# Performance work log

Hardware: AMD Instinct MI355X
Metric: run time of the kernel (lower is better)

## Reference

```python
import jax, jax.numpy as jnp
import numpy as np

EMBED = 1024
HEADS = 16
HEAD_DIM = EMBED // HEADS


def setup_inputs() -> dict:
    key = jax.random.key(0)
    ks = jax.random.split(key, 10)
    B, S = 2, 2048
    x = jax.random.normal(ks[0], (B, S, EMBED), dtype=jnp.float32)
    s = 1.0 / np.sqrt(EMBED)
    Wq = jax.random.normal(ks[1], (EMBED, EMBED), dtype=jnp.float32) * s
    Wk = jax.random.normal(ks[2], (EMBED, EMBED), dtype=jnp.float32) * s
    Wv = jax.random.normal(ks[3], (EMBED, EMBED), dtype=jnp.float32) * s
    Wo = jax.random.normal(ks[4], (EMBED, EMBED), dtype=jnp.float32) * s
    bq = jnp.zeros((EMBED,), jnp.float32)
    bk = jnp.zeros((EMBED,), jnp.float32)
    bv = jnp.zeros((EMBED,), jnp.float32)
    bo = jnp.zeros((EMBED,), jnp.float32)
    J = jax.random.normal(ks[5], (HEADS, HEAD_DIM, HEAD_DIM), dtype=jnp.float32) * 0.02
    lam = jnp.asarray(0.5, jnp.float32)
    return {"x": x, "Wq": Wq, "bq": bq, "Wk": Wk, "bk": bk,
            "Wv": Wv, "bv": bv, "Wo": Wo, "bo": bo, "J": J, "lam": lam}


def reference(x, Wq, bq, Wk, bk, Wv, bv, Wo, bo, J, lam):
    B, S, E = x.shape
    H, hd = HEADS, HEAD_DIM
    scale = np.sqrt(hd).astype(np.float32)

    def split_heads(t):  # (B,S,E) -> (B,H,S,hd)
        return t.reshape(B, S, H, hd).transpose(0, 2, 1, 3)

    Q = split_heads(x @ Wq + bq)
    K = split_heads(x @ Wk + bk)
    V = split_heads(x @ Wv + bv)

    scores = jnp.einsum('bhid,bhjd->bhij', Q, K) / scale
    Qn = jnp.tanh(Q)
    Kn = jnp.tanh(K)
    # bilinear correction: tanh(Q) J tanh(K)^T per head
    delta = jnp.einsum('bhid,hde,bhje->bhij', Qn, J, Kn)
    scores = scores + lam * delta

    causal = jnp.triu(jnp.ones((S, S), dtype=bool), k=1)  # True above diagonal
    scores = jnp.where(causal[None, None], -jnp.inf, scores)

    probs = jax.nn.softmax(scores, axis=-1)
    out = jnp.einsum('bhij,bhjd->bhid', probs, V)
    out = out.transpose(0, 2, 1, 3).reshape(B, S, E)
    return out @ Wo + bo
```

## Files before the change

kernel.cpp:

```cpp
#include <hip/hip_runtime.h>
#include <cstdint>
#include <cstddef>

typedef __bf16 bf16x8 __attribute__((ext_vector_type(8)));
typedef short  s16x8  __attribute__((ext_vector_type(8)));
typedef float  f32x4  __attribute__((ext_vector_type(4)));
typedef unsigned int u32x4 __attribute__((ext_vector_type(4)));
typedef unsigned int u32x2 __attribute__((ext_vector_type(2)));

#define MFMA16(a, b, c) __builtin_amdgcn_mfma_f32_16x16x32_bf16((a), (b), (c), 0, 0, 0)

typedef __attribute__((address_space(3))) unsigned int       lds_uint;
typedef const __attribute__((address_space(1))) unsigned int glb_uint;

static __device__ __forceinline__ void gload_lds16(const void* g, void* l) {
  __builtin_amdgcn_global_load_lds((glb_uint*)g, (lds_uint*)l, 16, 0, 0);
}

static __device__ __forceinline__ unsigned short f2bf(float f) {
  unsigned u = __builtin_bit_cast(unsigned, f);
  unsigned r = u + 0x7FFFu + ((u >> 16) & 1u);
  return (unsigned short)(r >> 16);
}
static __device__ __forceinline__ float bf2f(unsigned short u) {
  unsigned x = ((unsigned)u) << 16;
  return __builtin_bit_cast(float, x);
}
static __device__ __forceinline__ float fast_tanh(float x) {
  float e = __expf(2.f * x);
  return 1.f - 2.f / (e + 1.f);
}
static __device__ __forceinline__ unsigned cvt_pk_bf16(float lo, float hi) {
  unsigned r;
  asm("v_cvt_pk_bf16_f32 %0, %1, %2" : "=v"(r) : "v"(lo), "v"(hi));
  return r;
}
static __device__ __forceinline__ u32x4 tanh8(u32x4 q, float mul) {
  u32x4 o;
#pragma unroll
  for (int j = 0; j < 4; ++j) {
    float lo = bf2f((unsigned short)(q[j] & 0xffffu)) * mul;
    float hi = bf2f((unsigned short)(q[j] >> 16)) * mul;
    o[j] = cvt_pk_bf16(fast_tanh(lo), fast_tanh(hi));
  }
  return o;
}

__global__ void k_f32_to_bf16(const float* __restrict__ src,
                              unsigned short* __restrict__ dst, int n4) {
  int i = blockIdx.x * blockDim.x + threadIdx.x;
  if (i >= n4) return;
  float4 v = reinterpret_cast<const float4*>(src)[i];
  ushort4 o;
  o.x = f2bf(v.x); o.y = f2bf(v.y); o.z = f2bf(v.z); o.w = f2bf(v.w);
  reinterpret_cast<ushort4*>(dst)[i] = o;
}

__global__ void k_transpose4_to_bf16(const float* __restrict__ s0,
                                     const float* __restrict__ s1,
                                     const float* __restrict__ s2,
                                     const float* __restrict__ s3,
                                     unsigned short* __restrict__ dstBase) {
  __shared__ float t[32][33];
  const int z = blockIdx.z;
  const float* src = (z == 0) ? s0 : (z == 1) ? s1 : (z == 2) ? s2 : s3;
  unsigned short* dst = dstBase + (size_t)z * 1048576;
  int c0 = blockIdx.x * 32, r0 = blockIdx.y * 32;
  int tx = threadIdx.x, ty = threadIdx.y;
#pragma unroll
  for (int i = 0; i < 4; ++i)
    t[ty + i * 8][tx] = src[(size_t)(r0 + ty + i * 8) * 1024 + c0 + tx];
  __syncthreads();
#pragma unroll
  for (int i = 0; i < 4; ++i)
    dst[(size_t)(c0 + ty + i * 8) * 1024 + r0 + tx] = f2bf(t[tx][ty + i * 8]);
}

__global__ __launch_bounds__(256) void k_gemm_op(
    const unsigned short* __restrict__ A, const unsigned short* __restrict__ Bt,
    int M, int N, int K,
    float* __restrict__ Cout, const float* __restrict__ bias) {
  __shared__ __align__(16) unsigned short Al[2][128 * 64];
  __shared__ __align__(16) unsigned short Bl[2][128 * 64];
  const int tid = threadIdx.x;
  const int lane = tid & 63, w = tid >> 6;
  const int wm = w >> 1, wn = w & 1;
  const int l15 = lane & 15, l4 = lane >> 4;
  const int m0 = blockIdx.y * 128, n0 = blockIdx.x * 128;
  const int NT = K >> 6;

  const int srow = lane >> 3;
  const int schunk = (lane & 7) ^ srow;
  const unsigned short* Ag = A + (size_t)(m0 + (w << 5) + srow) * K + (schunk << 3);
  const unsigned short* Bg = Bt + (size_t)(n0 + (w << 5) + srow) * K + (schunk << 3);

  auto stage = [&](int slot, int t) {
    unsigned short* Alw = &Al[slot][0] + (w << 5) * 64;
    unsigned short* Blw = &Bl[slot][0] + (w << 5) * 64;
#pragma unroll
    for (int p = 0; p < 4; ++p) {
      gload_lds16(Ag + (size_t)(p * 8) * K + t * 64, Alw + p * 8 * 64);
      gload_lds16(Bg + (size_t)(p * 8) * K + t * 64, Blw + p * 8 * 64);
    }
  };

  const f32x4 zero4 = {0.f, 0.f, 0.f, 0.f};
  f32x4 acc[4][4];
#pragma unroll
  for (int i = 0; i < 4; ++i)
#pragma unroll
    for (int j = 0; j < 4; ++j) acc[i][j] = zero4;

  stage(0, 0);
  __syncthreads();

  for (int t = 0; t < NT; ++t) {
    const int s = t & 1;
    const int tn = (t + 1 < NT) ? t + 1 : NT - 1;
    stage(s ^ 1, tn);
    const char* As = (const char*)&Al[s][0];
    const char* Bs = (const char*)&Bl[s][0];
#pragma unroll
    for (int c = 0; c < 2; ++c) {
      bf16x8 af[4], bfr[4];
#pragma unroll
      for (int i = 0; i < 4; ++i) {
        int ra = wm * 64 + i * 16 + l15;
        af[i] = *reinterpret_cast<const bf16x8*>(
            As + ra * 128 + ((c * 64 + l4 * 16) ^ ((ra & 7) << 4)));
        int rb = wn * 64 + i * 16 + l15;
        bfr[i] = *reinterpret_cast<const bf16x8*>(
            Bs + rb * 128 + ((c * 64 + l4 * 16) ^ ((rb & 7) << 4)));
      }
      __builtin_amdgcn_s_setprio(1);
#pragma unroll
      for (int i = 0; i < 4; ++i)
#pragma unroll
        for (int j = 0; j < 4; ++j) acc[i][j] = MFMA16(af[i], bfr[j], acc[i][j]);
      __builtin_amdgcn_s_setprio(0);
    }
    __syncthreads();
  }

#pragma unroll
  for (int i = 0; i < 4; ++i)
#pragma unroll
    for (int j = 0; j < 4; ++j)
#pragma unroll
      for (int r = 0; r < 4; ++r) {
        int mrow = m0 + wm * 64 + i * 16 + l4 * 4 + r;
        int ncol = n0 + wn * 64 + j * 16 + l15;
        Cout[(size_t)mrow * N + ncol] = acc[i][j][r] + bias[ncol];
      }
}

__global__ __launch_bounds__(512, 2) void k_gemm256_qkv(
    const unsigned short* __restrict__ A, const unsigned short* __restrict__ Bt,
    int M, int N, int K,
    const float* __restrict__ bq, const float* __restrict__ bk,
    const float* __restrict__ bv,
    unsigned short* __restrict__ Qa, unsigned short* __restrict__ Ka,
    unsigned short* __restrict__ Vt, unsigned short* __restrict__ Qn) {
  __shared__ __align__(16) unsigned short SLDS[4 * 256 * 64];
  const int tid = threadIdx.x;
  const int lane = tid & 63;
  const int w = tid >> 6, wm = w >> 2, wn = w & 3;
  const int l15 = lane & 15, l4 = lane >> 4;
  const int nbx = N >> 8;
  const int bid = (int)blockIdx.x;
  const int lin = (bid & 7) * ((int)gridDim.x >> 3) + (bid >> 3);
  const int m0 = (lin / nbx) << 8, n0 = (lin % nbx) << 8;
  const int NT = K >> 6;

  const int strow = tid >> 3, stchunk = tid & 7;
  const int schunk = stchunk ^ (strow & 7);

  auto stage = [&](int slot, int kt) {
    unsigned short* Ad = SLDS + slot * 16384;
    unsigned short* Bd = SLDS + (2 + slot) * 16384;
#pragma unroll
    for (int i = 0; i < 4; ++i) {
      int row = i * 64 + strow;
      gload_lds16(A + (size_t)(m0 + row) * K + kt * 64 + schunk * 8,
                  Ad + row * 64 + stchunk * 8);
      gload_lds16(Bt + (size_t)(n0 + row) * K + kt * 64 + schunk * 8,
                  Bd + row * 64 + stchunk * 8);
    }
  };

  const f32x4 zero4 = {0.f, 0.f, 0.f, 0.f};
  f32x4 acc[8][4];
#pragma unroll
  for (int i = 0; i < 8; ++i)
#pragma unroll
    for (int j = 0; j < 4; ++j) acc[i][j] = zero4;

  stage(0, 0);
  __syncthreads();

  bf16x8 af[4][2], bf0[2][2], bf1[2][2];

  for (int kt = 0; kt < NT; ++kt) {
    const int s = kt & 1;
    const char* As = (const char*)(SLDS + s * 16384);
    const char* Bs = (const char*)(SLDS + (2 + s) * 16384);
    const int kp1 = (kt + 1 < NT) ? kt + 1 : NT - 1;

    stage(s ^ 1, kp1);

#pragma unroll
    for (int i = 0; i < 4; ++i) {
      const int ra = wm * 128 + i * 16 + l15;
#pragma unroll
      for (int kk = 0; kk < 2; ++kk)
        af[i][kk] = *(const bf16x8*)(As + ra * 128 + (((kk * 4 + l4) ^ (ra & 7)) << 4));
    }
#pragma unroll
    for (int j = 0; j < 2; ++j) {
      const int rb = wn * 64 + j * 16 + l15;
#pragma unroll
      for (int kk = 0; kk < 2; ++kk)
        bf0[j][kk] = *(const bf16x8*)(Bs + rb * 128 + (((kk * 4 + l4) ^ (rb & 7)) << 4));
    }
    __builtin_amdgcn_s_setprio(1);
#pragma unroll
    for (int i = 0; i < 4; ++i)
#pragma unroll
      for (int j = 0; j < 2; ++j)
#pragma unroll
        for (int kk = 0; kk < 2; ++kk)
          acc[i][j] = MFMA16(af[i][kk], bf0[j][kk], acc[i][j]);
    __builtin_amdgcn_s_setprio(0);

#pragma unroll
    for (int j = 0; j < 2; ++j) {
      const int rb = wn * 64 + (2 + j) * 16 + l15;
#pragma unroll
      for (int kk = 0; kk < 2; ++kk)
        bf1[j][kk] = *(const bf16x8*)(Bs + rb * 128 + (((kk * 4 + l4) ^ (rb & 7)) << 4));
    }
    __builtin_amdgcn_s_setprio(1);
#pragma unroll
    for (int i = 0; i < 4; ++i)
#pragma unroll
      for (int j = 0; j < 2; ++j)
#pragma unroll
        for (int kk = 0; kk < 2; ++kk)
          acc[i][2 + j] = MFMA16(af[i][kk], bf1[j][kk], acc[i][2 + j]);
    __builtin_amdgcn_s_setprio(0);

#pragma unroll
    for (int i = 0; i < 4; ++i) {
      const int ra = wm * 128 + (4 + i) * 16 + l15;
#pragma unroll
      for (int kk = 0; kk < 2; ++kk)
        af[i][kk] = *(const bf16x8*)(As + ra * 128 + (((kk * 4 + l4) ^ (ra & 7)) << 4));
    }
    __builtin_amdgcn_s_setprio(1);
#pragma unroll
    for (int i = 0; i < 4; ++i)
#pragma unroll
      for (int j = 0; j < 2; ++j)
#pragma unroll
        for (int kk = 0; kk < 2; ++kk)
          acc[4 + i][2 + j] = MFMA16(af[i][kk], bf1[j][kk], acc[4 + i][2 + j]);

#pragma unroll
    for (int i = 0; i < 4; ++i)
#pragma unroll
      for (int j = 0; j < 2; ++j)
#pragma unroll
        for (int kk = 0; kk < 2; ++kk)
          acc[4 + i][j] = MFMA16(af[i][kk], bf0[j][kk], acc[4 + i][j]);
    __builtin_amdgcn_s_setprio(0);

    __syncthreads();
  }

  char* wbuf = reinterpret_cast<char*>(SLDS) + w * 16384;
  const int proj = n0 >> 10;
  const int nn0 = (n0 + wn * 64) & 1023;
  const int hh = nn0 >> 6;
  const int mbase = m0 + wm * 128;
  const int bb = mbase >> 11;
  const float* bias = (proj == 0) ? bq : (proj == 1) ? bk : bv;
  float bcol[4];
#pragma unroll
  for (int nf = 0; nf < 4; ++nf) bcol[nf] = bias[nn0 + nf * 16 + l15];

  if (proj == 2) {
#pragma unroll
    for (int mf = 0; mf < 8; ++mf) {
#pragma unroll
      for (int nf = 0; nf < 4; ++nf) {
        const int d = nf * 16 + l15;
        const int tok = mf * 16 + l4 * 4;
        u32x2 pk;
        pk[0] = cvt_pk_bf16(acc[mf][nf][0] + bcol[nf], acc[mf][nf][1] + bcol[nf]);
        pk[1] = cvt_pk_bf16(acc[mf][nf][2] + bcol[nf], acc[mf][nf][3] + bcol[nf]);
        *reinterpret_cast<u32x2*>(
            wbuf + d * 256 + (((tok >> 3) ^ (d & 7)) << 4) + (tok & 7) * 2) = pk;
      }
    }
    __syncthreads();
    const size_t vbase = (size_t)(bb * 16 + hh) * 64 * 2048;
#pragma unroll
    for (int dblk = 0; dblk < 8; ++dblk) {
#pragma unroll
      for (int thalf = 0; thalf < 2; ++thalf) {
        const int d = (lane >> 3) + dblk * 8;
        const int tch = (lane & 7) + thalf * 8;
        u32x4 vv = *reinterpret_cast<const u32x4*>(
            wbuf + d * 256 + ((tch ^ (d & 7)) << 4));
        const int sidx = (mbase + tch * 8) & 2047;
        *reinterpret_cast<u32x4*>(Vt + vbase + (size_t)d * 2048 + sidx) = vv;
      }
    }
  } else {
#pragma unroll
    for (int mf = 0; mf < 8; ++mf) {
#pragma unroll
      for (int nf = 0; nf < 4; ++nf) {
        const int d = nf * 16 + l15;
#pragma unroll
        for (int r = 0; r < 4; ++r) {
          float v = acc[mf][nf][r] + bcol[nf];
          if (proj == 0) v *= 0.125f;
          const int tok = mf * 16 + l4 * 4 + r;
          *reinterpret_cast<unsigned short*>(wbuf + tok * 128 + d * 2) = f2bf(v);
        }
      }
    }
    __syncthreads();
    const size_t t64base = (size_t)(bb * 16 + hh) * 2048;
#pragma unroll
    for (int iter = 0; iter < 16; ++iter) {
      const int tl = (lane >> 3) + iter * 8;
      const int dc = lane & 7;
      u32x4 q8 = *reinterpret_cast<const u32x4*>(wbuf + tl * 128 + dc * 16);
      const size_t t64 = t64base + ((mbase + tl) & 2047);
      if (proj == 0) {
        *reinterpret_cast<u32x4*>(Qa + t64 * 128 + dc * 8) = q8;
        u32x4 qn = tanh8(q8, 8.0f);
        *reinterpret_cast<u32x4*>(Qn + t64 * 64 + dc * 8) = qn;
      } else {
        *reinterpret_cast<u32x4*>(Ka + t64 * 128 + dc * 8) = q8;
        u32x4 kn = tanh8(q8, 1.0f);
        *reinterpret_cast<u32x4*>(Ka + t64 * 128 + 64 + dc * 8) = kn;
      }
    }
  }
}

__global__ __launch_bounds__(256) void k_qnj(const unsigned short* __restrict__ Qn,
                                             const float* __restrict__ J,
                                             const float* __restrict__ lamPtr,
                                             unsigned short* __restrict__ Qa) {
  __shared__ float Jl[64 * 64];
  __shared__ float Ql[64 * 64];
  int bid = blockIdx.x;
  int bh = bid >> 5, sblk = bid & 31;
  int h = bh & 15;
  int tid = threadIdx.x;
  float lam = lamPtr[0];
  const float4* Jh = reinterpret_cast<const float4*>(J + (size_t)h * 4096);
#pragma unroll
  for (int p = 0; p < 4; ++p)
    reinterpret_cast<float4*>(Jl)[p * 256 + tid] = Jh[p * 256 + tid];
  size_t tok0 = (size_t)bh * 2048 + sblk * 64;
#pragma unroll
  for (int p = 0; p < 2; ++p) {
    int idx = p * 256 + tid;
    s16x8 v = *reinterpret_cast<const s16x8*>(Qn + tok0 * 64 + idx * 8);
#pragma unroll
    for (int j = 0; j < 8; ++j) Ql[idx * 8 + j] = bf2f((unsigned short)v[j]);
  }
  __syncthreads();
  int e = tid & 63, wq = tid >> 6;
#pragma unroll 1
  for (int pass = 0; pass < 16; ++pass) {
    int tok = pass * 4 + wq;
    float a0 = 0.f, a1 = 0.f;
#pragma unroll
    for (int d = 0; d < 64; d += 2) {
      a0 += Ql[tok * 64 + d] * Jl[d * 64 + e];
      a1 += Ql[tok * 64 + d + 1] * Jl[(d + 1) * 64 + e];
    }
    Qa[(tok0 + tok) * 128 + 64 + e] = f2bf(lam * (a0 + a1));
  }
}

__global__ __launch_bounds__(256) void k_attn(const unsigned short* __restrict__ Qa,
                                              const unsigned short* __restrict__ Ka,
                                              const unsigned short* __restrict__ Vt,
                                              unsigned short* __restrict__ Ob) {
  constexpr int S = 2048;
  __shared__ __align__(16) unsigned short Klds[2][64 * 128];
  __shared__ __align__(16) unsigned short Vtl[2][64 * 64];

  const int blk = (int)blockIdx.x;
  const int xg = blk & 7, idx = blk >> 3;
  const int bh = xg * 4 + (idx & 3);
  const int qt = 31 - (idx >> 2);
  const int b = bh >> 4, h = bh & 15;
  const int tid = threadIdx.x;
  const int lane = tid & 63, w = tid >> 6;
  const int l15 = lane & 15, l4 = lane >> 4;
  const int q0 = qt * 64;
  const size_t bhS = (size_t)bh * S;
  const unsigned short* Kbase = Ka + bhS * 128;
  const unsigned short* Vbase = Vt + (size_t)bh * 64 * 2048;
  const f32x4 zero4 = {0.f, 0.f, 0.f, 0.f};

  const int rowbase = w * 16 + (lane >> 4);
  const int rb7 = rowbase & 7;
  const int cK0 = (lane & 15) ^ rb7;
  const int cK1 = cK0 ^ 4;
  const int vdvrow = w * 16 + (lane >> 3);
  const int cV = (lane & 7) ^ ((lane >> 3) & 7);

  bf16x8 qf[4];
  {
    int qrow = q0 + w * 16 + l15;
#pragma unroll
    for (int c = 0; c < 4; ++c)
      qf[c] = *reinterpret_cast<const bf16x8*>(Qa + (bhS + qrow) * 128 + c * 32 + l4 * 8);
  }

  f32x4 oacc[4];
  float m_ = -__builtin_inff(), lsum = 0.f;
#pragma unroll
  for (int v = 0; v < 4; ++v) oacc[v] = zero4;

  const int I0 = (l15 + 32 * (l4 & 1)) * 4;
  const int I1 = I0 + 64;
  const bool hi4 = (lane & 32) != 0;

#pragma unroll
  for (int p = 0; p < 4; ++p)
    gload_lds16(Kbase + (size_t)(rowbase + 4 * p) * 128 + ((p & 1) ? cK1 : cK0) * 8,
                &Klds[0][(w * 16 + p * 4) * 128]);
#pragma unroll
  for (int p = 0; p < 2; ++p)
    gload_lds16(Vbase + (size_t)(vdvrow + 8 * p) * 2048 + cV * 8,
                &Vtl[0][(w * 16 + p * 8) * 64]);
  __syncthreads();

  for (int kt = 0; kt <= qt; ++kt) {
    const int cur = kt & 1;
    const bool lastStep = (kt == qt);

    if (!lastStep) {
      const int base = (kt + 1) * 64;
      const int nxt = cur ^ 1;
#pragma unroll
      for (int p = 0; p < 4; ++p)
        gload_lds16(Kbase + (size_t)(base + rowbase + 4 * p) * 128 + ((p & 1) ? cK1 : cK0) * 8,
                    &Klds[nxt][(w * 16 + p * 4) * 128]);
#pragma unroll
      for (int p = 0; p < 2; ++p)
        gload_lds16(Vbase + (size_t)(vdvrow + 8 * p) * 2048 + base + cV * 8,
                    &Vtl[nxt][(w * 16 + p * 8) * 64]);
    }

    const char* Kl = reinterpret_cast<const char*>(Klds[cur]);
    f32x4 sc[4];
    __builtin_amdgcn_s_setprio(1);
#pragma unroll
    for (int fn = 0; fn < 4; ++fn) {
      sc[fn] = zero4;
      const int krow = fn * 16 + l15;
#pragma unroll
      for (int c = 0; c < 4; ++c) {
        bf16x8 kf = *reinterpret_cast<const bf16x8*>(
            Kl + krow * 256 + (((c * 4 + l4) ^ (krow & 7)) << 4));
        sc[fn] = MFMA16(kf, qf[c], sc[fn]);
      }
    }
    __builtin_amdgcn_s_setprio(0);

    if (lastStep) {
      const int qloc = w * 16 + l15;
#pragma unroll
      for (int fn = 0; fn < 4; ++fn)
#pragma unroll
        for (int r = 0; r < 4; ++r)
          if (fn * 16 + l4 * 4 + r > qloc) sc[fn][r] = -__builtin_inff();
    }

    float mx = sc[0][0];
#pragma unroll
    for (int fn = 0; fn < 4; ++fn)
#pragma unroll
      for (int r = 0; r < 4; ++r) mx = fmaxf(mx, sc[fn][r]);
    mx = fmaxf(mx, __shfl_xor(mx, 16));
    mx = fmaxf(mx, __shfl_xor(mx, 32));
    const float mn = fmaxf(m_, mx);
    const float al = __expf(m_ - mn);
    float p_[4][4];
    float rs = 0.f;
#pragma unroll
    for (int fn = 0; fn < 4; ++fn)
#pragma unroll
      for (int r = 0; r < 4; ++r) {
        float e = __expf(sc[fn][r] - mn);
        p_[fn][r] = e;
        rs += e;
      }
    rs += __shfl_xor(rs, 16);
    rs += __shfl_xor(rs, 32);
    lsum = lsum * al + rs;
    m_ = mn;

#pragma unroll
    for (int r = 0; r < 4; ++r) {
      float albc = __shfl(al, l4 * 4 + r);
#pragma unroll
      for (int v = 0; v < 4; ++v) oacc[v][r] *= albc;
    }

    unsigned cp[4][2];
#pragma unroll
    for (int fn = 0; fn < 4; ++fn) {
      cp[fn][0] = cvt_pk_bf16(p_[fn][0], p_[fn][1]);
      cp[fn][1] = cvt_pk_bf16(p_[fn][2], p_[fn][3]);
    }

    const char* Vl = reinterpret_cast<const char*>(Vtl[cur]);
#pragma unroll
    for (int c2 = 0; c2 < 2; ++c2) {
      unsigned a0 = __builtin_amdgcn_ds_bpermute(I0, (int)cp[c2 * 2][0]);
      unsigned b0 = __builtin_amdgcn_ds_bpermute(I0, (int)cp[c2 * 2 + 1][0]);
      unsigned a1 = __builtin_amdgcn_ds_bpermute(I0, (int)cp[c2 * 2][1]);
      unsigned b1 = __builtin_amdgcn_ds_bpermute(I0, (int)cp[c2 * 2 + 1][1]);
      unsigned a2 = __builtin_amdgcn_ds_bpermute(I1, (int)cp[c2 * 2][0]);
      unsigned b2 = __builtin_amdgcn_ds_bpermute(I1, (int)cp[c2 * 2 + 1][0]);
      unsigned a3 = __builtin_amdgcn_ds_bpermute(I1, (int)cp[c2 * 2][1]);
      unsigned b3 = __builtin_amdgcn_ds_bpermute(I1, (int)cp[c2 * 2 + 1][1]);
      u32x4 pw = {hi4 ? b0 : a0, hi4 ? b1 : a1, hi4 ? b2 : a2, hi4 ? b3 : a3};
      bf16x8 pa = __builtin_bit_cast(bf16x8, pw);
      __builtin_amdgcn_s_setprio(1);
#pragma unroll
      for (int v = 0; v < 4; ++v) {
        const int dvrow = v * 16 + l15;
        bf16x8 vf = *reinterpret_cast<const bf16x8*>(
            Vl + dvrow * 128 + (((c2 * 4 + l4) ^ (dvrow & 7)) << 4));
        oacc[v] = MFMA16(pa, vf, oacc[v]);
      }
      __builtin_amdgcn_s_setprio(0);
    }

    __syncthreads();
  }

  float lbc[4];
#pragma unroll
  for (int r = 0; r < 4; ++r) lbc[r] = __shfl(lsum, l4 * 4 + r);
#pragma unroll
  for (int v = 0; v < 4; ++v) {
#pragma unroll
    for (int r = 0; r < 4; ++r) {
      int row = q0 + w * 16 + l4 * 4 + r;
      float o = oacc[v][r] / lbc[r];
      Ob[((size_t)b * S + row) * 1024 + h * 64 + v * 16 + l15] = f2bf(o);
    }
  }
}

extern "C" void kernel_launch(void* const* d_in, const int* in_sizes, int n_in,
                              void* d_out, int out_size, void* d_ws, size_t ws_size,
                              hipStream_t stream) {
  const float* x   = (const float*)d_in[0];
  const float* Wq  = (const float*)d_in[1];
  const float* bq  = (const float*)d_in[2];
  const float* Wk  = (const float*)d_in[3];
  const float* bk  = (const float*)d_in[4];
  const float* Wv  = (const float*)d_in[5];
  const float* bv  = (const float*)d_in[6];
  const float* Wo  = (const float*)d_in[7];
  const float* bo  = (const float*)d_in[8];
  const float* J   = (const float*)d_in[9];
  const float* lam = (const float*)d_in[10];
  float* out = (float*)d_out;

  char* ws = (char*)d_ws;
  unsigned short* xb     = (unsigned short*)(ws);
  unsigned short* Wt_qkv = (unsigned short*)(ws + 8388608);
  unsigned short* Wt_o   = (unsigned short*)(ws + 14680064);
  unsigned short* Qa     = (unsigned short*)(ws + 16777216);
  unsigned short* Ka     = (unsigned short*)(ws + 33554432);
  unsigned short* Vt     = (unsigned short*)(ws + 50331648);
  unsigned short* Qn     = (unsigned short*)(ws + 58720256);
  unsigned short* Ob     = (unsigned short*)(ws + 67108864);

  k_f32_to_bf16<<<4096, 256, 0, stream>>>(x, xb, 1048576);

  k_transpose4_to_bf16<<<dim3(32, 32, 4), dim3(32, 8), 0, stream>>>(
      Wq, Wk, Wv, Wo, Wt_qkv);

  k_gemm256_qkv<<<192, 512, 0, stream>>>(xb, Wt_qkv, 4096, 3072, 1024,
      bq, bk, bv, Qa, Ka, Vt, Qn);

  k_qnj<<<1024, 256, 0, stream>>>(Qn, J, lam, Qa);

  k_attn<<<1024, 256, 0, stream>>>(Qa, Ka, Vt, Ob);

  k_gemm_op<<<dim3(8, 32), 256, 0, stream>>>(Ob, Wt_o, 4096, 1024, 1024,
      out, bo);
}
```

Measured before the change: 159.6 us.

## Process 128 query rows per attention block to reuse K/V tiles

Each attention workgroup now handles a 128-row query tile, with every wave owning two 16-row sub-tiles, instead of a 64-row tile. Each K and V tile loaded into LDS feeds twice as many MFMAs, which halves global-to-LDS traffic and the per-tile synchronisation overhead. The grid shrinks from 1024 to 512 blocks and register use rises with the doubled accumulators, which can lower occupancy and worsen load balance across CUs. The causal mask is now applied per sub-tile whenever a key tile overlaps it.

```diff
diff --git a/kernel.cpp b/kernel.cpp
--- a/kernel.cpp
+++ b/kernel.cpp
@@ -401,12 +401,13 @@
   const int blk = (int)blockIdx.x;
   const int xg = blk & 7, idx = blk >> 3;
   const int bh = xg * 4 + (idx & 3);
-  const int qt = 31 - (idx >> 2);
+  const int qt = 15 - (idx >> 2);
   const int b = bh >> 4, h = bh & 15;
   const int tid = threadIdx.x;
   const int lane = tid & 63, w = tid >> 6;
   const int l15 = lane & 15, l4 = lane >> 4;
-  const int q0 = qt * 64;
+  const int q0 = qt * 128;
+  const int NT = 2 * qt + 2;
   const size_t bhS = (size_t)bh * S;
   const unsigned short* Kbase = Ka + bhS * 128;
   const unsigned short* Vbase = Vt + (size_t)bh * 64 * 2048;
@@ -419,18 +420,23 @@
   const int vdvrow = w * 16 + (lane >> 3);
   const int cV = (lane & 7) ^ ((lane >> 3) & 7);
 
-  bf16x8 qf[4];
-  {
-    int qrow = q0 + w * 16 + l15;
+  bf16x8 qf[2][4];
+#pragma unroll
+  for (int qs = 0; qs < 2; ++qs) {
+    int qrow = q0 + w * 32 + qs * 16 + l15;
 #pragma unroll
     for (int c = 0; c < 4; ++c)
-      qf[c] = *reinterpret_cast<const bf16x8*>(Qa + (bhS + qrow) * 128 + c * 32 + l4 * 8);
-  }
-
-  f32x4 oacc[4];
-  float m_ = -__builtin_inff(), lsum = 0.f;
-#pragma unroll
-  for (int v = 0; v < 4; ++v) oacc[v] = zero4;
+      qf[qs][c] = *reinterpret_cast<const bf16x8*>(Qa + (bhS + qrow) * 128 + c * 32 + l4 * 8);
+  }
+
+  f32x4 oacc[2][4];
+  float m_[2], lsum[2];
+#pragma unroll
+  for (int qs = 0; qs < 2; ++qs) {
+    m_[qs] = -__builtin_inff(); lsum[qs] = 0.f;
+#pragma unroll
+    for (int v = 0; v < 4; ++v) oacc[qs][v] = zero4;
+  }
 
   const int I0 = (l15 + 32 * (l4 & 1)) * 4;
   const int I1 = I0 + 64;
@@ -446,11 +452,10 @@
                 &Vtl[0][(w * 16 + p * 8) * 64]);
   __syncthreads();
 
-  for (int kt = 0; kt <= qt; ++kt) {
+  for (int kt = 0; kt < NT; ++kt) {
     const int cur = kt & 1;
-    const bool lastStep = (kt == qt);
-
-    if (!lastStep) {
+
+    if (kt + 1 < NT) {
       const int base = (kt + 1) * 64;
       const int nxt = cur ^ 1;
 #pragma unroll
@@ -464,88 +469,95 @@
     }
 
     const char* Kl = reinterpret_cast<const char*>(Klds[cur]);
-    f32x4 sc[4];
+    f32x4 sc[2][4];
     __builtin_amdgcn_s_setprio(1);
 #pragma unroll
     for (int fn = 0; fn < 4; ++fn) {
-      sc[fn] = zero4;
+      sc[0][fn] = zero4; sc[1][fn] = zero4;
       const int krow = fn * 16 + l15;
 #pragma unroll
       for (int c = 0; c < 4; ++c) {
         bf16x8 kf = *reinterpret_cast<const bf16x8*>(
             Kl + krow * 256 + (((c * 4 + l4) ^ (krow & 7)) << 4));
-        sc[fn] = MFMA16(kf, qf[c], sc[fn]);
+        sc[0][fn] = MFMA16(kf, qf[0][c], sc[0][fn]);
+        sc[1][fn] = MFMA16(kf, qf[1][c], sc[1][fn]);
       }
     }
     __builtin_amdgcn_s_setprio(0);
 
-    if (lastStep) {
-      const int qloc = w * 16 + l15;
+    unsigned cp[2][4][2];
+#pragma unroll
+    for (int qs = 0; qs < 2; ++qs) {
+      const int qmin = q0 + w * 32 + qs * 16;
+      if (kt * 64 + 63 > qmin) {
+        const int qloc = qmin + l15;
+#pragma unroll
+        for (int fn = 0; fn < 4; ++fn)
+#pragma unroll
+          for (int r = 0; r < 4; ++r)
+            if (kt * 64 + fn * 16 + l4 * 4 + r > qloc) sc[qs][fn][r] = -__builtin_inff();
+      }
+      float mx = sc[qs][0][0];
 #pragma unroll
       for (int fn = 0; fn < 4; ++fn)
 #pragma unroll
-        for (int r = 0; r < 4; ++r)
-          if (fn * 16 + l4 * 4 + r > qloc) sc[fn][r] = -__builtin_inff();
-    }
-
-    float mx = sc[0][0];
-#pragma unroll
-    for (int fn = 0; fn < 4; ++fn)
-#pragma unroll
-      for (int r = 0; r < 4; ++r) mx = fmaxf(mx, sc[fn][r]);
-    mx = fmaxf(mx, __shfl_xor(mx, 16));
-    mx = fmaxf(mx, __shfl_xor(mx, 32));
-    const float mn = fmaxf(m_, mx);
-    const float al = __expf(m_ - mn);
-    float p_[4][4];
-    float rs = 0.f;
-#pragma unroll
-    for (int fn = 0; fn < 4; ++fn)
+        for (int r = 0; r < 4; ++r) mx = fmaxf(mx, sc[qs][fn][r]);
+      mx = fmaxf(mx, __shfl_xor(mx, 16));
+      mx = fmaxf(mx, __shfl_xor(mx, 32));
+      const float mn = fmaxf(m_[qs], mx);
+      const float al = __expf(m_[qs] - mn);
+      float p_[4][4];
+      float rs = 0.f;
+#pragma unroll
+      for (int fn = 0; fn < 4; ++fn)
+#pragma unroll
+        for (int r = 0; r < 4; ++r) {
+          float e = __expf(sc[qs][fn][r] - mn);
+          p_[fn][r] = e;
+          rs += e;
+        }
+      rs += __shfl_xor(rs, 16);
+      rs += __shfl_xor(rs, 32);
+      lsum[qs] = lsum[qs] * al + rs;
+      m_[qs] = mn;
 #pragma unroll
       for (int r = 0; r < 4; ++r) {
-        float e = __expf(sc[fn][r] - mn);
-        p_[fn][r] = e;
-        rs += e;
-      }
-    rs += __shfl_xor(rs, 16);
-    rs += __shfl_xor(rs, 32);
-    lsum = lsum * al + rs;
-    m_ = mn;
-
-#pragma unroll
-    for (int r = 0; r < 4; ++r) {
-      float albc = __shfl(al, l4 * 4 + r);
-#pragma unroll
-      for (int v = 0; v < 4; ++v) oacc[v][r] *= albc;
-    }
-
-    unsigned cp[4][2];
-#pragma unroll
-    for (int fn = 0; fn < 4; ++fn) {
-      cp[fn][0] = cvt_pk_bf16(p_[fn][0], p_[fn][1]);
-      cp[fn][1] = cvt_pk_bf16(p_[fn][2], p_[fn][3]);
+        float albc = __shfl(al, l4 * 4 + r);
+#pragma unroll
+        for (int v = 0; v < 4; ++v) oacc[qs][v][r] *= albc;
+      }
+#pragma unroll
+      for (int fn = 0; fn < 4; ++fn) {
+        cp[qs][fn][0] = cvt_pk_bf16(p_[fn][0], p_[fn][1]);
+        cp[qs][fn][1] = cvt_pk_bf16(p_[fn][2], p_[fn][3]);
+      }
     }
 
     const char* Vl = reinterpret_cast<const char*>(Vtl[cur]);
 #pragma unroll
     for (int c2 = 0; c2 < 2; ++c2) {
-      unsigned a0 = __builtin_amdgcn_ds_bpermute(I0, (int)cp[c2 * 2][0]);
-      unsigned b0 = __builtin_amdgcn_ds_bpermute(I0, (int)cp[c2 * 2 + 1][0]);
-      unsigned a1 = __builtin_amdgcn_ds_bpermute(I0, (int)cp[c2 * 2][1]);
-      unsigned b1 = __builtin_amdgcn_ds_bpermute(I0, (int)cp[c2 * 2 + 1][1]);
-      unsigned a2 = __builtin_amdgcn_ds_bpermute(I1, (int)cp[c2 * 2][0]);
-      unsigned b2 = __builtin_amdgcn_ds_bpermute(I1, (int)cp[c2 * 2 + 1][0]);
-      unsigned a3 = __builtin_amdgcn_ds_bpermute(I1, (int)cp[c2 * 2][1]);
-      unsigned b3 = __builtin_amdgcn_ds_bpermute(I1, (int)cp[c2 * 2 + 1][1]);
-      u32x4 pw = {hi4 ? b0 : a0, hi4 ? b1 : a1, hi4 ? b2 : a2, hi4 ? b3 : a3};
-      bf16x8 pa = __builtin_bit_cast(bf16x8, pw);
+      bf16x8 pa[2];
+#pragma unroll
+      for (int qs = 0; qs < 2; ++qs) {
+        unsigned a0 = __builtin_amdgcn_ds_bpermute(I0, (int)cp[qs][c2 * 2][0]);
+        unsigned b0 = __builtin_amdgcn_ds_bpermute(I0, (int)cp[qs][c2 * 2 + 1][0]);
+        unsigned a1 = __builtin_amdgcn_ds_bpermute(I0, (int)cp[qs][c2 * 2][1]);
+        unsigned b1 = __builtin_amdgcn_ds_bpermute(I0, (int)cp[qs][c2 * 2 + 1][1]);
+        unsigned a2 = __builtin_amdgcn_ds_bpermute(I1, (int)cp[qs][c2 * 2][0]);
+        unsigned b2 = __builtin_amdgcn_ds_bpermute(I1, (int)cp[qs][c2 * 2 + 1][0]);
+        unsigned a3 = __builtin_amdgcn_ds_bpermute(I1, (int)cp[qs][c2 * 2][1]);
+        unsigned b3 = __builtin_amdgcn_ds_bpermute(I1, (int)cp[qs][c2 * 2 + 1][1]);
+        u32x4 pw = {hi4 ? b0 : a0, hi4 ? b1 : a1, hi4 ? b2 : a2, hi4 ? b3 : a3};
+        pa[qs] = __builtin_bit_cast(bf16x8, pw);
+      }
       __builtin_amdgcn_s_setprio(1);
 #pragma unroll
       for (int v = 0; v < 4; ++v) {
         const int dvrow = v * 16 + l15;
         bf16x8 vf = *reinterpret_cast<const bf16x8*>(
             Vl + dvrow * 128 + (((c2 * 4 + l4) ^ (dvrow & 7)) << 4));
-        oacc[v] = MFMA16(pa, vf, oacc[v]);
+        oacc[0][v] = MFMA16(pa[0], vf, oacc[0][v]);
+        oacc[1][v] = MFMA16(pa[1], vf, oacc[1][v]);
       }
       __builtin_amdgcn_s_setprio(0);
     }
@@ -553,16 +565,19 @@
     __syncthreads();
   }
 
-  float lbc[4];
-#pragma unroll
-  for (int r = 0; r < 4; ++r) lbc[r] = __shfl(lsum, l4 * 4 + r);
-#pragma unroll
-  for (int v = 0; v < 4; ++v) {
-#pragma unroll
-    for (int r = 0; r < 4; ++r) {
-      int row = q0 + w * 16 + l4 * 4 + r;
-      float o = oacc[v][r] / lbc[r];
-      Ob[((size_t)b * S + row) * 1024 + h * 64 + v * 16 + l15] = f2bf(o);
+#pragma unroll
+  for (int qs = 0; qs < 2; ++qs) {
+    float lbc[4];
+#pragma unroll
+    for (int r = 0; r < 4; ++r) lbc[r] = __shfl(lsum[qs], l4 * 4 + r);
+#pragma unroll
+    for (int v = 0; v < 4; ++v) {
+#pragma unroll
+      for (int r = 0; r < 4; ++r) {
+        int row = q0 + w * 32 + qs * 16 + l4 * 4 + r;
+        float o = oacc[qs][v][r] / lbc[r];
+        Ob[((size_t)b * S + row) * 1024 + h * 64 + v * 16 + l15] = f2bf(o);
+      }
     }
   }
 }
@@ -603,7 +618,7 @@
 
   k_qnj<<<1024, 256, 0, stream>>>(Qn, J, lam, Qa);
 
-  k_attn<<<1024, 256, 0, stream>>>(Qa, Ka, Vt, Ob);
+  k_attn<<<512, 256, 0, stream>>>(Qa, Ka, Vt, Ob);
 
   k_gemm_op<<<dim3(8, 32), 256, 0, stream>>>(Ob, Wt_o, 4096, 1024, 1024,
       out, bo);
```

After: 178.5 us. +11.9%, slower.
